# Performance work log

Hardware: AMD Instinct MI355X
Metric: run time of the kernel (lower is better)

## Reference

```python
import jax, jax.numpy as jnp
import numpy as np

# Mamba2 default hyperparameters
D_MODEL = 768
EXPAND = 2
D_STATE = 128
D_CONV = 4
HEADDIM = 64
D_INNER = EXPAND * D_MODEL            # 1536
NHEADS = D_INNER // HEADDIM           # 24
CONV_DIM = D_INNER + 2 * D_STATE      # 1792 (ngroups=1)
D_IN_PROJ = 2 * D_INNER + 2 * D_STATE + NHEADS  # 3352
B = 4
L = 2048
EPS = 1e-5


def setup_inputs() -> dict:
    key = jax.random.key(0)
    ks = jax.random.split(key, 8)
    return {
        "x": jax.random.normal(ks[0], (B, L, D_MODEL), jnp.float32),
        "in_proj_w": jax.random.normal(ks[1], (D_IN_PROJ, D_MODEL), jnp.float32) * 0.02,
        "conv_w": jax.random.normal(ks[2], (CONV_DIM, D_CONV), jnp.float32) * 0.2,
        "conv_b": jnp.zeros((CONV_DIM,), jnp.float32),
        # inverse-softplus of dt in [1e-3, 0.1] (Mamba2 dt init)
        "dt_bias": jnp.log(jnp.expm1(jax.random.uniform(ks[3], (NHEADS,), jnp.float32, 1e-3, 0.1))),
        "A_log": jnp.log(jax.random.uniform(ks[4], (NHEADS,), jnp.float32, 1.0, 16.0)),
        "D": jnp.ones((NHEADS,), jnp.float32),
        "norm_w": jnp.ones((D_INNER,), jnp.float32),
        "out_proj_w": jax.random.normal(ks[5], (D_MODEL, D_INNER), jnp.float32) * 0.02,
    }


def _mamba2(x, in_proj_w, conv_w, conv_b, dt_bias, A_log, D, norm_w, out_proj_w):
    b, l, _ = x.shape
    zxbcdt = x @ in_proj_w.T                              # (b,l,D_IN_PROJ)
    z, xBC, dt = jnp.split(zxbcdt, [D_INNER, D_INNER + CONV_DIM], axis=-1)

    # causal depthwise conv1d over channels of xBC, kernel D_CONV
    xp = jnp.pad(xBC, ((0, 0), (D_CONV - 1, 0), (0, 0)))
    conv = conv_b + sum(xp[:, k:k + l, :] * conv_w[:, k] for k in range(D_CONV))
    xBC = jax.nn.silu(conv)

    xh, Bm, Cm = jnp.split(xBC, [D_INNER, D_INNER + D_STATE], axis=-1)
    xh = xh.reshape(b, l, NHEADS, HEADDIM)               # (b,l,h,p)

    dt = jax.nn.softplus(dt + dt_bias)                   # (b,l,h)
    A = -jnp.exp(A_log)                                  # (h,)
    dA = jnp.exp(dt * A)                                 # (b,l,h)

    # selective SSM scan over time (state: (b,h,p,n))
    def step(state, inp):
        dA_t, dt_t, x_t, B_t, C_t = inp
        state = state * dA_t[:, :, None, None] \
              + (dt_t[:, :, None] * x_t)[..., None] * B_t[:, None, None, :]
        y_t = jnp.einsum('bhpn,bn->bhp', state, C_t)
        return state, y_t

    state0 = jnp.zeros((b, NHEADS, HEADDIM, D_STATE), x.dtype)
    xs = (dA.transpose(1, 0, 2), dt.transpose(1, 0, 2),
          xh.transpose(1, 0, 2, 3), Bm.transpose(1, 0, 2), Cm.transpose(1, 0, 2))
    _, ys = jax.lax.scan(step, state0, xs)               # (l,b,h,p)
    y = ys.transpose(1, 0, 2, 3) + D[:, None] * xh       # D skip connection
    y = y.reshape(b, l, D_INNER)

    # gated RMSNorm (norm_before_gate=False): normalize after gating by silu(z)
    y = y * jax.nn.silu(z)
    y = y * jax.lax.rsqrt(jnp.mean(y * y, axis=-1, keepdims=True) + EPS) * norm_w
    return y @ out_proj_w.T


def reference(x, in_proj_w, conv_w, conv_b, dt_bias, A_log, D, norm_w, out_proj_w):
    # MambaBlock.forward: Mamba2(x) + x
    return _mamba2(x, in_proj_w, conv_w, conv_b, dt_bias, A_log, D, norm_w, out_proj_w) + x
```

## Files before the change

### kernel.cpp

```cpp
#include <hip/hip_runtime.h>
#include <math.h>

typedef __bf16 bf16x8 __attribute__((ext_vector_type(8)));
typedef float  f32x4  __attribute__((ext_vector_type(4)));

#define QCHUNK 128
#define NCHUNK 16
#define SLD 136

__device__ __forceinline__ float bf2f(unsigned short u) {
    union { unsigned int i; float f; } v; v.i = ((unsigned int)u) << 16; return v.f;
}
__device__ __forceinline__ unsigned short f2bf(float f) {
    union { float f; unsigned int i; } v; v.f = f;
    unsigned int x = v.i;
    unsigned int r = (x + 0x7FFFu + ((x >> 16) & 1u)) >> 16;
    return (unsigned short)r;
}
__device__ __forceinline__ uint4 pack8(float4 a, float4 b) {
    uint4 r;
    r.x = (unsigned)f2bf(a.x) | ((unsigned)f2bf(a.y) << 16);
    r.y = (unsigned)f2bf(a.z) | ((unsigned)f2bf(a.w) << 16);
    r.z = (unsigned)f2bf(b.x) | ((unsigned)f2bf(b.y) << 16);
    r.w = (unsigned)f2bf(b.z) | ((unsigned)f2bf(b.w) << 16);
    return r;
}
__device__ __forceinline__ void load_lds16(const void* g, void* l) {
    __builtin_amdgcn_global_load_lds((const __attribute__((address_space(1))) void*)g,
                                     (__attribute__((address_space(3))) void*)l,
                                     16, 0, 0);
}

__global__ __launch_bounds__(256)
void convert_kernel(const float* __restrict__ x, const float* __restrict__ w_in,
                    const float* __restrict__ w_out,
                    unsigned short* __restrict__ x_bf, unsigned short* __restrict__ w_in_bf,
                    unsigned short* __restrict__ w_out_bf) {
    int idx = blockIdx.x * 256 + threadIdx.x;
    const int NX  = 8192 * 768 / 8;
    const int NW1 = 3328 * 768 / 8;
    const int NW2 = 768 * 1536 / 8;
    if (idx < NX) {
        const float* s = x + (size_t)idx * 8;
        *(uint4*)(x_bf + (size_t)idx * 8) = pack8(*(const float4*)s, *(const float4*)(s + 4));
    } else if (idx < NX + NW1) {
        int j = idx - NX;
        const float* s = w_in + (size_t)j * 8;
        *(uint4*)(w_in_bf + (size_t)j * 8) = pack8(*(const float4*)s, *(const float4*)(s + 4));
    } else if (idx < NX + NW1 + NW2) {
        int j = idx - NX - NW1;
        const float* s = w_out + (size_t)j * 8;
        *(uint4*)(w_out_bf + (size_t)j * 8) = pack8(*(const float4*)s, *(const float4*)(s + 4));
    }
}

__global__ __launch_bounds__(512)
void gemm_8phase(const unsigned short* __restrict__ A,
                 const unsigned short* __restrict__ Bw,
                 unsigned short* __restrict__ Out,
                 int ldo, int K) {
    extern __shared__ __align__(16) char smem[];

    const int tid = threadIdx.x;
    const int bid = blockIdx.x;
    const int xcd = bid & 7, local = bid >> 3;
    const int mt = xcd * 4 + local / 13;
    const int nt = local % 13;
    const int m0 = mt * 256, n0 = nt * 256;

    const int wave = tid >> 6, lane = tid & 63;
    const int wr = wave >> 2, wc = wave & 3;
    const int lr = lane & 15, q = lane >> 4;

    const int gl   = (lr & 7) << 4;
    const int arow = wr * 128 + lr;
    const int brow = wc * 64 + lr;
    const int colq = q << 4;

    const int srow  = tid >> 3;
    const int sslot = (tid & 7) ^ (srow & 7);
    const unsigned short* ga = A  + (size_t)(m0 + srow) * K + sslot * 8;
    const unsigned short* gb = Bw + (size_t)(n0 + srow) * K + sslot * 8;
    char* sAd = smem +         (size_t)tid * 16;
    char* sBd = smem + 65536 + (size_t)tid * 16;
    const size_t gstep = (size_t)64 * K;

    const int NT = K >> 6;
    f32x4 acc[8][4] = {};

    #pragma unroll
    for (int i = 0; i < 4; ++i) {
        load_lds16(ga + (size_t)i * gstep, sAd + i * 8192);
        load_lds16(gb + (size_t)i * gstep, sBd + i * 8192);
    }

    for (int t = 0; t < NT; ++t) {
        const int d = t & 1;
        const bool more = (t + 1 < NT);
        if (more) {
            const size_t kg = (size_t)(t + 1) * 64;
            const int ld = (d ^ 1) * 32768;
            #pragma unroll
            for (int i = 0; i < 4; ++i) {
                load_lds16(ga + kg + (size_t)i * gstep, sAd + ld + i * 8192);
                load_lds16(gb + kg + (size_t)i * gstep, sBd + ld + i * 8192);
            }
            asm volatile("s_waitcnt vmcnt(8)" ::: "memory");
        } else {
            asm volatile("s_waitcnt vmcnt(0)" ::: "memory");
        }
        __builtin_amdgcn_s_barrier();

        const char* pa = smem +         d * 32768;
        const char* pb = smem + 65536 + d * 32768;
        #pragma unroll
        for (int kh = 0; kh < 2; ++kh) {
            const int col = ((kh << 6) | colq) ^ gl;
            bf16x8 af[8], bfr[4];
            #pragma unroll
            for (int m = 0; m < 8; ++m)
                af[m] = *(const bf16x8*)(pa + (arow + m * 16) * 128 + col);
            #pragma unroll
            for (int n = 0; n < 4; ++n)
                bfr[n] = *(const bf16x8*)(pb + (brow + n * 16) * 128 + col);

            __builtin_amdgcn_s_setprio(1);
            #pragma unroll
            for (int m = 0; m < 8; ++m)
                #pragma unroll
                for (int n = 0; n < 4; ++n)
                    acc[m][n] = __builtin_amdgcn_mfma_f32_16x16x32_bf16(af[m], bfr[n], acc[m][n], 0, 0, 0);
            __builtin_amdgcn_s_setprio(0);
        }
        __builtin_amdgcn_s_barrier();
    }

    #pragma unroll
    for (int m = 0; m < 8; ++m) {
        #pragma unroll
        for (int r = 0; r < 4; ++r) {
            int row = m0 + wr * 128 + m * 16 + q * 4 + r;
            #pragma unroll
            for (int n = 0; n < 4; ++n) {
                int col = n0 + wc * 64 + n * 16 + lr;
                Out[(size_t)row * ldo + col] = f2bf(acc[m][n][r]);
            }
        }
    }
}

__global__ __launch_bounds__(512)
void gemm_out(const unsigned short* __restrict__ A,
              const unsigned short* __restrict__ Bw,
              float* __restrict__ Out, const float* __restrict__ Resid,
              int lda) {
    extern __shared__ __align__(16) char smem[];
    const int K = 1536, Nn = 768;

    const int tid = threadIdx.x;
    const int bid = blockIdx.x;
    const int xcd = bid & 7, local = bid >> 3;
    const int mt = xcd * 8 + local / 6;
    const int nt = local % 6;
    const int m0 = mt * 128, n0 = nt * 128;

    const int wave = tid >> 6, lane = tid & 63;
    const int wr = wave >> 2, wc = wave & 3;
    const int lr = lane & 15, q = lane >> 4;

    const int gl   = (lr & 7) << 4;
    const int arow = wr * 64 + lr;
    const int brow = wc * 32 + lr;
    const int colq = q << 4;

    const int srow  = tid >> 3;
    const int sslot = (tid & 7) ^ (srow & 7);
    const unsigned short* ga = A  + (size_t)(m0 + srow) * lda + sslot * 8;
    const unsigned short* gb = Bw + (size_t)(n0 + srow) * K   + sslot * 8;
    char* sAd = smem +         (size_t)tid * 16;
    char* sBd = smem + 32768 + (size_t)tid * 16;
    const size_t gstep_a = (size_t)64 * lda;
    const size_t gstep_b = (size_t)64 * K;

    f32x4 acc[4][2] = {};

    #pragma unroll
    for (int i = 0; i < 2; ++i) {
        load_lds16(ga + (size_t)i * gstep_a, sAd + i * 8192);
        load_lds16(gb + (size_t)i * gstep_b, sBd + i * 8192);
    }

    const int NT = K >> 6;
    for (int t = 0; t < NT; ++t) {
        const int d = t & 1;
        const bool more = (t + 1 < NT);
        if (more) {
            const size_t kg = (size_t)(t + 1) * 64;
            const int ld = (d ^ 1) * 16384;
            #pragma unroll
            for (int i = 0; i < 2; ++i) {
                load_lds16(ga + kg + (size_t)i * gstep_a, sAd + ld + i * 8192);
                load_lds16(gb + kg + (size_t)i * gstep_b, sBd + ld + i * 8192);
            }
            asm volatile("s_waitcnt vmcnt(4)" ::: "memory");
        } else {
            asm volatile("s_waitcnt vmcnt(0)" ::: "memory");
        }
        __builtin_amdgcn_s_barrier();

        const char* pa = smem +         d * 16384;
        const char* pb = smem + 32768 + d * 16384;
        #pragma unroll
        for (int kh = 0; kh < 2; ++kh) {
            const int col = ((kh << 6) | colq) ^ gl;
            bf16x8 af[4], bfr[2];
            #pragma unroll
            for (int m = 0; m < 4; ++m)
                af[m] = *(const bf16x8*)(pa + (arow + m * 16) * 128 + col);
            #pragma unroll
            for (int n = 0; n < 2; ++n)
                bfr[n] = *(const bf16x8*)(pb + (brow + n * 16) * 128 + col);

            __builtin_amdgcn_s_setprio(1);
            #pragma unroll
            for (int m = 0; m < 4; ++m)
                #pragma unroll
                for (int n = 0; n < 2; ++n)
                    acc[m][n] = __builtin_amdgcn_mfma_f32_16x16x32_bf16(af[m], bfr[n], acc[m][n], 0, 0, 0);
            __builtin_amdgcn_s_setprio(0);
        }
        __builtin_amdgcn_s_barrier();
    }

    #pragma unroll
    for (int m = 0; m < 4; ++m) {
        #pragma unroll
        for (int r = 0; r < 4; ++r) {
            int row = m0 + wr * 64 + m * 16 + q * 4 + r;
            #pragma unroll
            for (int n = 0; n < 2; ++n) {
                int col = n0 + wc * 32 + n * 16 + lr;
                Out[(size_t)row * Nn + col] = acc[m][n][r] + Resid[(size_t)row * Nn + col];
            }
        }
    }
}

__global__ __launch_bounds__(256)
void conv_fused_kernel(const unsigned short* __restrict__ zx,
                       const float* __restrict__ cw, const float* __restrict__ cb,
                       unsigned short* __restrict__ xT, unsigned short* __restrict__ bT,
                       unsigned short* __restrict__ Brow, unsigned short* __restrict__ Crow) {
    __shared__ unsigned short outt[64][66];
    __shared__ float cwl[64][4];
    __shared__ float cbl[64];

    int blk = blockIdx.x;
    int cht = blk % 28;
    int tt  = (blk / 28) % 32;
    int b   = blk / (28 * 32);
    int ch0 = cht * 64, t0 = tt * 64;
    int tid = threadIdx.x;
    int tx = tid & 63, ty = tid >> 6;

    if (tid < 64) cbl[tid] = cb[ch0 + tid];
    cwl[tid >> 2][tid & 3] = cw[(ch0 + (tid >> 2)) * 4 + (tid & 3)];
    __syncthreads();

    const unsigned short* zp = zx + (size_t)(b * 2048) * 3352 + 1536 + ch0 + tx;
    float w0 = cwl[tx][0], w1 = cwl[tx][1], w2 = cwl[tx][2], w3 = cwl[tx][3];
    float bias = cbl[tx];
    int tg = t0 + ty * 16;
    float r0 = (tg >= 3) ? bf2f(zp[(size_t)(tg - 3) * 3352]) : 0.f;
    float r1 = (tg >= 2) ? bf2f(zp[(size_t)(tg - 2) * 3352]) : 0.f;
    float r2 = (tg >= 1) ? bf2f(zp[(size_t)(tg - 1) * 3352]) : 0.f;
    #pragma unroll
    for (int k = 0; k < 16; ++k) {
        float cur = bf2f(zp[(size_t)(tg + k) * 3352]);
        float a = bias + r0 * w0 + r1 * w1 + r2 * w2 + cur * w3;
        a = a / (1.f + __expf(-a));
        outt[ty * 16 + k][tx] = f2bf(a);
        r0 = r1; r1 = r2; r2 = cur;
    }
    __syncthreads();

    if (ch0 < 1536) {
        unsigned short* dst = xT + ((size_t)(b * 1536 + ch0)) * 2048 + t0;
        #pragma unroll
        for (int k = 0; k < 16; ++k) {
            int chl = ty * 16 + k;
            dst[(size_t)chl * 2048 + tx] = outt[tx][chl];
        }
    } else if (ch0 < 1664) {
        int n0 = ch0 - 1536;
        unsigned short* dstT = bT + ((size_t)(b * 128 + n0)) * 2048 + t0;
        #pragma unroll
        for (int k = 0; k < 16; ++k) {
            int chl = ty * 16 + k;
            dstT[(size_t)chl * 2048 + tx] = outt[tx][chl];
        }
        unsigned short* dstR = Brow + ((size_t)(b * 2048 + t0)) * 128 + n0;
        int tl = tid >> 3, c8 = (tid & 7) << 3;
        #pragma unroll
        for (int it = 0; it < 2; ++it) {
            int t = tl + it * 32;
            unsigned short tmp[8];
            #pragma unroll
            for (int jj = 0; jj < 8; ++jj) tmp[jj] = outt[t][c8 + jj];
            *(uint4*)(dstR + (size_t)t * 128 + c8) = *(uint4*)tmp;
        }
    } else {
        int n0 = ch0 - 1664;
        unsigned short* dstR = Crow + ((size_t)(b * 2048 + t0)) * 128 + n0;
        int tl = tid >> 3, c8 = (tid & 7) << 3;
        #pragma unroll
        for (int it = 0; it < 2; ++it) {
            int t = tl + it * 32;
            unsigned short tmp[8];
            #pragma unroll
            for (int jj = 0; jj < 8; ++jj) tmp[jj] = outt[t][c8 + jj];
            *(uint4*)(dstR + (size_t)t * 128 + c8) = *(uint4*)tmp;
        }
    }
}

__global__ __launch_bounds__(256)
void dt_kernel(const float* __restrict__ x, const float* __restrict__ w_in,
               const float* __restrict__ dt_bias, const float* __restrict__ A_log,
               float2* __restrict__ dtdA) {
    __shared__ float xs[8 * 768];
    __shared__ float wsh[24 * 257];
    const int tid = threadIdx.x;
    const int row0 = blockIdx.x * 8;

    for (int i = tid; i < 8 * 768 / 4; i += 256)
        *(float4*)(xs + i * 4) = *(const float4*)(x + (size_t)row0 * 768 + (size_t)i * 4);

    const int rr = tid / 24, hh = tid - rr * 24;
    float acc0 = 0.f, acc1 = 0.f, acc2 = 0.f, acc3 = 0.f;

    for (int kc = 0; kc < 3; ++kc) {
        __syncthreads();
        for (int i = tid; i < 24 * 256; i += 256) {
            int h = i >> 8, kk = i & 255;
            wsh[h * 257 + kk] = w_in[(size_t)(3328 + h) * 768 + kc * 256 + kk];
        }
        __syncthreads();
        if (tid < 192) {
            const float* xp = xs + rr * 768 + kc * 256;
            const float* wp = wsh + hh * 257;
            #pragma unroll 16
            for (int kk = 0; kk < 256; kk += 4) {
                acc0 += xp[kk]     * wp[kk];
                acc1 += xp[kk + 1] * wp[kk + 1];
                acc2 += xp[kk + 2] * wp[kk + 2];
                acc3 += xp[kk + 3] * wp[kk + 3];
            }
        }
    }
    if (tid < 192) {
        float v = (acc0 + acc1) + (acc2 + acc3) + dt_bias[hh];
        float dt = (v > 20.f) ? v : log1pf(expf(v));
        float A = -expf(A_log[hh]);
        dtdA[(size_t)(row0 + rr) * 24 + hh] = make_float2(dt, dt * A);
    }
}

__global__ __launch_bounds__(256)
void ssd_local_kernel(const unsigned short* __restrict__ Brow,
                      const unsigned short* __restrict__ Crow,
                      const float2* __restrict__ dtdA,
                      const unsigned short* __restrict__ xT,
                      const unsigned short* __restrict__ bT,
                      const float* __restrict__ Dh,
                      unsigned short* __restrict__ yb,
                      unsigned short* __restrict__ sst,
                      float* __restrict__ Pbuf) {
    extern __shared__ __align__(16) char smem[];
    __bf16* Bs  = (__bf16*)smem;
    __bf16* Cs  = (__bf16*)(smem + 34816);
    float*  Lc  = (float*)(smem + 69632);
    float*  dtl = (float*)(smem + 70144);

    const int tid = threadIdx.x;
    const int c   = blockIdx.x & 15;
    const int bh  = blockIdx.x >> 4;
    const int b   = bh / 24, h = bh % 24;
    const int t0g = b * 2048 + c * QCHUNK;
    const int wave = tid >> 6, lane = tid & 63;
    const int lr = lane & 15, q = lane >> 4;

    for (int cc = tid; cc < 2048; cc += 256) {
        int r = cc >> 4, c8 = (cc & 15) << 3;
        *(uint4*)(Bs + r * SLD + c8) = *(const uint4*)(Brow + ((size_t)(t0g + r)) * 128 + c8);
        *(uint4*)(Cs + r * SLD + c8) = *(const uint4*)(Crow + ((size_t)(t0g + r)) * 128 + c8);
    }
    if (tid < 128) {
        float2 dd = dtdA[((size_t)t0g + tid) * 24 + h];
        dtl[tid] = dd.x;
        Lc[tid]  = dd.y;
    }
    __syncthreads();
    if (tid < 64) {
        float a0 = Lc[2 * tid], a1 = Lc[2 * tid + 1];
        float s = a0 + a1;
        #pragma unroll
        for (int d = 1; d < 64; d <<= 1) {
            float v = __shfl_up(s, d);
            if (tid >= d) s += v;
        }
        float ex = s - (a0 + a1);
        Lc[2 * tid]     = ex + a0;
        Lc[2 * tid + 1] = ex + a0 + a1;
    }
    __syncthreads();

    const int wm = (wave & 1) * 64, wn = (wave >> 1) * 64;
    f32x4 g[4][4] = {};
    #pragma unroll
    for (int k0 = 0; k0 < 128; k0 += 32) {
        bf16x8 af[4], bfr[4];
        #pragma unroll
        for (int t = 0; t < 4; ++t) {
            af[t]  = *(const bf16x8*)(Cs + (wm + t * 16 + lr) * SLD + k0 + q * 8);
            bfr[t] = *(const bf16x8*)(Bs + (wn + t * 16 + lr) * SLD + k0 + q * 8);
        }
        #pragma unroll
        for (int ti = 0; ti < 4; ++ti)
            #pragma unroll
            for (int tj = 0; tj < 4; ++tj)
                g[ti][tj] = __builtin_amdgcn_mfma_f32_16x16x32_bf16(af[ti], bfr[tj], g[ti][tj], 0, 0, 0);
    }
    __syncthreads();

    __bf16* Ms = Cs;
    {
        float lt_[4], dt_[4];
        #pragma unroll
        for (int tj = 0; tj < 4; ++tj) {
            int tau = wn + tj * 16 + lr;
            lt_[tj] = Lc[tau];
            dt_[tj] = dtl[tau];
        }
        #pragma unroll
        for (int ti = 0; ti < 4; ++ti) {
            #pragma unroll
            for (int r = 0; r < 4; ++r) {
                int t = wm + ti * 16 + q * 4 + r;
                float Lt = Lc[t];
                #pragma unroll
                for (int tj = 0; tj < 4; ++tj) {
                    int tau = wn + tj * 16 + lr;
                    float mv = (tau <= t) ? g[ti][tj][r] * __expf(Lt - lt_[tj]) * dt_[tj] : 0.f;
                    unsigned short u = f2bf(mv);
                    Ms[t * SLD + tau] = *(__bf16*)&u;
                }
            }
        }
    }

    __bf16* Xt  = Bs;
    __bf16* Xtw = (__bf16*)(smem + 17408);
    {
        float LQ = Lc[127];
        const unsigned short* xTb = xT + ((size_t)(b * 1536 + h * 64)) * 2048 + c * QCHUNK;
        for (int cc = tid; cc < 1024; cc += 256) {
            int p = cc >> 4, c8 = (cc & 15) << 3;
            uint4 v = *(const uint4*)(xTb + (size_t)p * 2048 + c8);
            *(uint4*)(Xt + p * SLD + c8) = v;
            unsigned short uu[8] = {(unsigned short)(v.x & 0xFFFF), (unsigned short)(v.x >> 16),
                                    (unsigned short)(v.y & 0xFFFF), (unsigned short)(v.y >> 16),
                                    (unsigned short)(v.z & 0xFFFF), (unsigned short)(v.z >> 16),
                                    (unsigned short)(v.w & 0xFFFF), (unsigned short)(v.w >> 16)};
            float w0[8];
            #pragma unroll
            for (int jj = 0; jj < 8; ++jj) {
                int tau = c8 + jj;
                w0[jj] = bf2f(uu[jj]) * __expf(LQ - Lc[tau]) * dtl[tau];
            }
            *(uint4*)(Xtw + p * SLD + c8) = pack8(make_float4(w0[0], w0[1], w0[2], w0[3]),
                                                  make_float4(w0[4], w0[5], w0[6], w0[7]));
        }
    }
    __syncthreads();

    {
        f32x4 so[2][4] = {};
        const unsigned short* bTb = bT + ((size_t)(b * 128)) * 2048 + c * QCHUNK;
        #pragma unroll
        for (int k0 = 0; k0 < 128; k0 += 32) {
            bf16x8 af[2], bfr[4];
            #pragma unroll
            for (int ti = 0; ti < 2; ++ti) {
                int n = wave * 32 + ti * 16 + lr;
                af[ti] = *(const bf16x8*)(bTb + (size_t)n * 2048 + k0 + q * 8);
            }
            #pragma unroll
            for (int tj = 0; tj < 4; ++tj)
                bfr[tj] = *(const bf16x8*)(Xtw + (tj * 16 + lr) * SLD + k0 + q * 8);
            #pragma unroll
            for (int ti = 0; ti < 2; ++ti)
                #pragma unroll
                for (int tj = 0; tj < 4; ++tj)
                    so[ti][tj] = __builtin_amdgcn_mfma_f32_16x16x32_bf16(af[ti], bfr[tj], so[ti][tj], 0, 0, 0);
        }
        unsigned short* sb = sst + ((size_t)(bh * NCHUNK + c)) * 8192;
        #pragma unroll
        for (int ti = 0; ti < 2; ++ti) {
            #pragma unroll
            for (int r = 0; r < 4; ++r) {
                int n = wave * 32 + ti * 16 + q * 4 + r;
                #pragma unroll
                for (int tj = 0; tj < 4; ++tj) {
                    int p = tj * 16 + lr;
                    sb[n * 64 + p] = f2bf(so[ti][tj][r]);
                }
            }
        }
        if (tid == 0) Pbuf[bh * NCHUNK + c] = __expf(Lc[127]);
    }

    {
        f32x4 ya[2][4] = {};
        #pragma unroll
        for (int k0 = 0; k0 < 128; k0 += 32) {
            bf16x8 af[2], bfr[4];
            #pragma unroll
            for (int ti = 0; ti < 2; ++ti)
                af[ti] = *(const bf16x8*)(Ms + (wave * 32 + ti * 16 + lr) * SLD + k0 + q * 8);
            #pragma unroll
            for (int tj = 0; tj < 4; ++tj)
                bfr[tj] = *(const bf16x8*)(Xt + (tj * 16 + lr) * SLD + k0 + q * 8);
            #pragma unroll
            for (int ti = 0; ti < 2; ++ti)
                #pragma unroll
                for (int tj = 0; tj < 4; ++tj)
                    ya[ti][tj] = __builtin_amdgcn_mfma_f32_16x16x32_bf16(af[ti], bfr[tj], ya[ti][tj], 0, 0, 0);
        }
        float Dv = Dh[h];
        unsigned short* ybb = yb + (size_t)t0g * 1536 + h * 64;
        #pragma unroll
        for (int ti = 0; ti < 2; ++ti) {
            #pragma unroll
            for (int r = 0; r < 4; ++r) {
                int t = wave * 32 + ti * 16 + q * 4 + r;
                #pragma unroll
                for (int tj = 0; tj < 4; ++tj) {
                    int p = tj * 16 + lr;
                    __bf16 xb = Xt[p * SLD + t];
                    float xv = bf2f(*(unsigned short*)&xb);
                    ybb[(size_t)t * 1536 + p] = f2bf(ya[ti][tj][r] + Dv * xv);
                }
            }
        }
    }
}

__global__ __launch_bounds__(256)
void combine_kernel(const unsigned short* __restrict__ sst,
                    unsigned short* __restrict__ sstT,
                    const float* __restrict__ Pbuf) {
    __shared__ unsigned short tl[32 * 130];
    const int blk = blockIdx.x;
    const int bh = blk >> 1;
    const int ph = (blk & 1) * 32;
    const int tid = threadIdx.x;
    const int pl = tid & 31;
    const int nb = tid >> 5;
    const unsigned short* sb = sst + (size_t)bh * NCHUNK * 8192;
    unsigned short* tb = sstT + (size_t)bh * NCHUNK * 8192 + ph * 128;
    const float* Pb = Pbuf + bh * NCHUNK;

    float s[16];
    #pragma unroll
    for (int i = 0; i < 16; ++i) s[i] = 0.f;

    for (int c = 0; c < NCHUNK; ++c) {
        const float Pc = Pb[c];
        const unsigned short* sc = sb + (size_t)c * 8192;
        #pragma unroll
        for (int i = 0; i < 16; ++i) {
            int n = nb + 8 * i;
            unsigned short v = sc[n * 64 + ph + pl];
            tl[pl * 130 + n] = f2bf(s[i]);
            s[i] = Pc * s[i] + bf2f(v);
        }
        __syncthreads();
        uint* tlw = (uint*)tl;
        uint4* tc4 = (uint4*)(tb + (size_t)c * 8192);
        #pragma unroll
        for (int k = 0; k < 2; ++k) {
            int j = tid + k * 256;
            int pp = j >> 4;
            int w0 = pp * 65 + (j & 15) * 4;
            tc4[j] = make_uint4(tlw[w0], tlw[w0 + 1], tlw[w0 + 2], tlw[w0 + 3]);
        }
        __syncthreads();
    }
}

__global__ __launch_bounds__(256)
void ssd_inter_kernel(const unsigned short* __restrict__ Crow,
                      const float2* __restrict__ dtdA,
                      const unsigned short* __restrict__ sstT,
                      unsigned short* __restrict__ yb) {
    __shared__ __align__(16) __bf16 Cs[128 * SLD];
    __shared__ __align__(16) __bf16 St[64 * SLD];
    __shared__ float Lc[128];

    const int tid = threadIdx.x;
    const int blk = blockIdx.x;
    const int bh = blk / 15;
    const int c  = blk % 15 + 1;
    const int b = bh / 24, h = bh % 24;
    const int t0g = b * 2048 + c * QCHUNK;
    const int wave = tid >> 6, lane = tid & 63;
    const int lr = lane & 15, q = lane >> 4;

    for (int cc = tid; cc < 2048; cc += 256) {
        int r = cc >> 4, c8 = (cc & 15) << 3;
        *(uint4*)(Cs + r * SLD + c8) = *(const uint4*)(Crow + ((size_t)(t0g + r)) * 128 + c8);
    }
    const unsigned short* stb = sstT + ((size_t)(bh * NCHUNK + c)) * 8192;
    for (int cc = tid; cc < 1024; cc += 256) {
        int p = cc >> 4, c8 = (cc & 15) << 3;
        *(uint4*)(St + p * SLD + c8) = *(const uint4*)(stb + p * 128 + c8);
    }
    if (tid < 128) Lc[tid] = dtdA[((size_t)t0g + tid) * 24 + h].y;
    __syncthreads();
    if (tid < 64) {
        float a0 = Lc[2 * tid], a1 = Lc[2 * tid + 1];
        float s = a0 + a1;
        #pragma unroll
        for (int d = 1; d < 64; d <<= 1) {
            float v = __shfl_up(s, d);
            if (tid >= d) s += v;
        }
        float ex = s - (a0 + a1);
        Lc[2 * tid]     = ex + a0;
        Lc[2 * tid + 1] = ex + a0 + a1;
    }
    __syncthreads();

    f32x4 ya[2][4] = {};
    #pragma unroll
    for (int k0 = 0; k0 < 128; k0 += 32) {
        bf16x8 af[2], bfr[4];
        #pragma unroll
        for (int ti = 0; ti < 2; ++ti)
            af[ti] = *(const bf16x8*)(Cs + (wave * 32 + ti * 16 + lr) * SLD + k0 + q * 8);
        #pragma unroll
        for (int tj = 0; tj < 4; ++tj)
            bfr[tj] = *(const bf16x8*)(St + (tj * 16 + lr) * SLD + k0 + q * 8);
        #pragma unroll
        for (int ti = 0; ti < 2; ++ti)
            #pragma unroll
            for (int tj = 0; tj < 4; ++tj)
                ya[ti][tj] = __builtin_amdgcn_mfma_f32_16x16x32_bf16(af[ti], bfr[tj], ya[ti][tj], 0, 0, 0);
    }
    unsigned short* ybb = yb + (size_t)t0g * 1536 + h * 64;
    #pragma unroll
    for (int ti = 0; ti < 2; ++ti) {
        #pragma unroll
        for (int r = 0; r < 4; ++r) {
            int t = wave * 32 + ti * 16 + q * 4 + r;
            float sc = __expf(Lc[t]);
            #pragma unroll
            for (int tj = 0; tj < 4; ++tj) {
                int p = tj * 16 + lr;
                unsigned short* yp = ybb + (size_t)t * 1536 + p;
                *yp = f2bf(bf2f(*yp) + sc * ya[ti][tj][r]);
            }
        }
    }
}

__global__ __launch_bounds__(256)
void norm_kernel(const unsigned short* __restrict__ yb,
                 unsigned short* __restrict__ zx,
                 const float* __restrict__ nw) {
    int row = blockIdx.x;
    const unsigned short* yr = yb + (size_t)row * 1536;
    unsigned short* zr = zx + (size_t)row * 3352;
    int tid = threadIdx.x;
    float u[6];
    float ss = 0.f;
    #pragma unroll
    for (int i = 0; i < 6; ++i) {
        int c = tid + i * 256;
        float z = bf2f(zr[c]);
        float uu = bf2f(yr[c]) * (z / (1.f + __expf(-z)));
        u[i] = uu;
        ss += uu * uu;
    }
    #pragma unroll
    for (int m = 1; m < 64; m <<= 1) ss += __shfl_xor(ss, m);
    __shared__ float red[4];
    if ((tid & 63) == 0) red[tid >> 6] = ss;
    __syncthreads();
    float tot = red[0] + red[1] + red[2] + red[3];
    float inv = rsqrtf(tot * (1.f / 1536.f) + 1e-5f);
    #pragma unroll
    for (int i = 0; i < 6; ++i) {
        int c = tid + i * 256;
        zr[1536 + c] = f2bf(u[i] * inv * nw[c]);
    }
}

extern "C" void kernel_launch(void* const* d_in, const int* in_sizes, int n_in,
                              void* d_out, int out_size, void* d_ws, size_t ws_size,
                              hipStream_t stream) {
    const float* x       = (const float*)d_in[0];
    const float* w_in    = (const float*)d_in[1];
    const float* conv_w  = (const float*)d_in[2];
    const float* conv_b  = (const float*)d_in[3];
    const float* dt_bias = (const float*)d_in[4];
    const float* A_log   = (const float*)d_in[5];
    const float* Dp      = (const float*)d_in[6];
    const float* nw      = (const float*)d_in[7];
    const float* w_out   = (const float*)d_in[8];
    float* out = (float*)d_out;

    char* ws = (char*)d_ws;
    const size_t off_zx   = 0;
    const size_t off_A    = off_zx + 54919168;
    const size_t off_xT   = off_A;
    const size_t off_bT   = off_A + 25165824;
    const size_t off_Brow = off_A + 27262976;
    const size_t off_Crow = off_A + 29360128;
    const size_t off_dtdA = off_A + 58720256;
    const size_t off_y    = off_dtdA + 1572864;
    const size_t off_sst  = off_y + 50331648;
    const size_t off_P    = off_sst + 25165824;

    unsigned short* zx   = (unsigned short*)(ws + off_zx);
    unsigned short* xT   = (unsigned short*)(ws + off_xT);
    unsigned short* bT   = (unsigned short*)(ws + off_bT);
    unsigned short* Brow = (unsigned short*)(ws + off_Brow);
    unsigned short* Crow = (unsigned short*)(ws + off_Crow);
    float2* dtdA = (float2*)(ws + off_dtdA);
    unsigned short* yb   = (unsigned short*)(ws + off_y);
    unsigned short* sst  = (unsigned short*)(ws + off_sst);
    unsigned short* sstT = xT;
    float* Pbuf = (float*)(ws + off_P);

    unsigned short* x_bf     = (unsigned short*)(ws + off_y);
    unsigned short* w_out_bf = (unsigned short*)(ws + off_y + 25165824);
    unsigned short* w_in_bf  = (unsigned short*)(ws + off_sst);

    static bool attr_set = false;
    if (!attr_set) {
        hipFuncSetAttribute((const void*)ssd_local_kernel,
                            hipFuncAttributeMaxDynamicSharedMemorySize, 70656);
        hipFuncSetAttribute((const void*)gemm_8phase,
                            hipFuncAttributeMaxDynamicSharedMemorySize, 131072);
        hipFuncSetAttribute((const void*)gemm_out,
                            hipFuncAttributeMaxDynamicSharedMemorySize, 65536);
        attr_set = true;
    }

    convert_kernel<<<4896, 256, 0, stream>>>(x, w_in, w_out, x_bf, w_in_bf, w_out_bf);
    gemm_8phase<<<416, 512, 131072, stream>>>(x_bf, w_in_bf, zx, 3352, 768);
    conv_fused_kernel<<<3584, 256, 0, stream>>>(zx, conv_w, conv_b, xT, bT, Brow, Crow);
    dt_kernel<<<1024, 256, 0, stream>>>(x, w_in, dt_bias, A_log, dtdA);
    ssd_local_kernel<<<1536, 256, 70656, stream>>>(Brow, Crow, dtdA, xT, bT, Dp, yb, sst, Pbuf);
    combine_kernel<<<192, 256, 0, stream>>>(sst, sstT, Pbuf);
    ssd_inter_kernel<<<1440, 256, 0, stream>>>(Crow, dtdA, sstT, yb);
    norm_kernel<<<8192, 256, 0, stream>>>(yb, zx, nw);
    gemm_out<<<384, 512, 65536, stream>>>(zx + 1536, w_out_bf, out, x, 3352);
}
```

Before: 318.9 us.

## Shrink SSD local kernel LDS by staging B in halves and folding decay weights into bT

Cuts the ssd_local_kernel shared memory from about 69KB to 53KB. B is now staged in two 64-column halves through a smaller buffer, and the CB^T GEMM is split into two K passes with an extra sync between them. The separate decay-weighted X tile in LDS is dropped; the exp(LQ-L)*dt weights are applied in registers to the bT fragments loaded from global. The goal is to fit more blocks per CU, at the cost of extra syncs and the weight exp computed redundantly per wave.

```diff
diff --git a/kernel.cpp b/kernel.cpp
--- a/kernel.cpp
+++ b/kernel.cpp
@@ -7,6 +7,7 @@
 #define QCHUNK 128
 #define NCHUNK 16
 #define SLD 136
+#define SLDB 72
 
 __device__ __forceinline__ float bf2f(unsigned short u) {
     union { unsigned int i; float f; } v; v.i = ((unsigned int)u) << 16; return v.f;
@@ -377,10 +378,10 @@
                       unsigned short* __restrict__ sst,
                       float* __restrict__ Pbuf) {
     extern __shared__ __align__(16) char smem[];
-    __bf16* Bs  = (__bf16*)smem;
-    __bf16* Cs  = (__bf16*)(smem + 34816);
-    float*  Lc  = (float*)(smem + 69632);
-    float*  dtl = (float*)(smem + 70144);
+    __bf16* Bh  = (__bf16*)smem;
+    __bf16* Cs  = (__bf16*)(smem + 18432);
+    float*  Lc  = (float*)(smem + 53248);
+    float*  dtl = (float*)(smem + 53760);
 
     const int tid = threadIdx.x;
     const int c   = blockIdx.x & 15;
@@ -392,8 +393,11 @@
 
     for (int cc = tid; cc < 2048; cc += 256) {
         int r = cc >> 4, c8 = (cc & 15) << 3;
-        *(uint4*)(Bs + r * SLD + c8) = *(const uint4*)(Brow + ((size_t)(t0g + r)) * 128 + c8);
         *(uint4*)(Cs + r * SLD + c8) = *(const uint4*)(Crow + ((size_t)(t0g + r)) * 128 + c8);
+    }
+    for (int cc = tid; cc < 1024; cc += 256) {
+        int r = cc >> 3, c8 = (cc & 7) << 3;
+        *(uint4*)(Bh + r * SLDB + c8) = *(const uint4*)(Brow + ((size_t)(t0g + r)) * 128 + c8);
     }
     if (tid < 128) {
         float2 dd = dtdA[((size_t)t0g + tid) * 24 + h];
@@ -401,6 +405,7 @@
         Lc[tid]  = dd.y;
     }
     __syncthreads();
+
     if (tid < 64) {
         float a0 = Lc[2 * tid], a1 = Lc[2 * tid + 1];
         float s = a0 + a1;
@@ -413,17 +418,36 @@
         Lc[2 * tid]     = ex + a0;
         Lc[2 * tid + 1] = ex + a0 + a1;
     }
-    __syncthreads();
 
     const int wm = (wave & 1) * 64, wn = (wave >> 1) * 64;
     f32x4 g[4][4] = {};
     #pragma unroll
-    for (int k0 = 0; k0 < 128; k0 += 32) {
+    for (int k0 = 0; k0 < 64; k0 += 32) {
         bf16x8 af[4], bfr[4];
         #pragma unroll
         for (int t = 0; t < 4; ++t) {
             af[t]  = *(const bf16x8*)(Cs + (wm + t * 16 + lr) * SLD + k0 + q * 8);
-            bfr[t] = *(const bf16x8*)(Bs + (wn + t * 16 + lr) * SLD + k0 + q * 8);
+            bfr[t] = *(const bf16x8*)(Bh + (wn + t * 16 + lr) * SLDB + k0 + q * 8);
+        }
+        #pragma unroll
+        for (int ti = 0; ti < 4; ++ti)
+            #pragma unroll
+            for (int tj = 0; tj < 4; ++tj)
+                g[ti][tj] = __builtin_amdgcn_mfma_f32_16x16x32_bf16(af[ti], bfr[tj], g[ti][tj], 0, 0, 0);
+    }
+    __syncthreads();
+    for (int cc = tid; cc < 1024; cc += 256) {
+        int r = cc >> 3, c8 = (cc & 7) << 3;
+        *(uint4*)(Bh + r * SLDB + c8) = *(const uint4*)(Brow + ((size_t)(t0g + r)) * 128 + 64 + c8);
+    }
+    __syncthreads();
+    #pragma unroll
+    for (int k0 = 0; k0 < 64; k0 += 32) {
+        bf16x8 af[4], bfr[4];
+        #pragma unroll
+        for (int t = 0; t < 4; ++t) {
+            af[t]  = *(const bf16x8*)(Cs + (wm + t * 16 + lr) * SLD + 64 + k0 + q * 8);
+            bfr[t] = *(const bf16x8*)(Bh + (wn + t * 16 + lr) * SLDB + k0 + q * 8);
         }
         #pragma unroll
         for (int ti = 0; ti < 4; ++ti)
@@ -459,45 +483,40 @@
         }
     }
 
-    __bf16* Xt  = Bs;
-    __bf16* Xtw = (__bf16*)(smem + 17408);
+    __bf16* Xt = Bh;
     {
-        float LQ = Lc[127];
         const unsigned short* xTb = xT + ((size_t)(b * 1536 + h * 64)) * 2048 + c * QCHUNK;
         for (int cc = tid; cc < 1024; cc += 256) {
             int p = cc >> 4, c8 = (cc & 15) << 3;
-            uint4 v = *(const uint4*)(xTb + (size_t)p * 2048 + c8);
-            *(uint4*)(Xt + p * SLD + c8) = v;
-            unsigned short uu[8] = {(unsigned short)(v.x & 0xFFFF), (unsigned short)(v.x >> 16),
-                                    (unsigned short)(v.y & 0xFFFF), (unsigned short)(v.y >> 16),
-                                    (unsigned short)(v.z & 0xFFFF), (unsigned short)(v.z >> 16),
-                                    (unsigned short)(v.w & 0xFFFF), (unsigned short)(v.w >> 16)};
-            float w0[8];
-            #pragma unroll
-            for (int jj = 0; jj < 8; ++jj) {
-                int tau = c8 + jj;
-                w0[jj] = bf2f(uu[jj]) * __expf(LQ - Lc[tau]) * dtl[tau];
-            }
-            *(uint4*)(Xtw + p * SLD + c8) = pack8(make_float4(w0[0], w0[1], w0[2], w0[3]),
-                                                  make_float4(w0[4], w0[5], w0[6], w0[7]));
+            *(uint4*)(Xt + p * SLD + c8) = *(const uint4*)(xTb + (size_t)p * 2048 + c8);
         }
     }
     __syncthreads();
 
     {
+        float LQ = Lc[127];
         f32x4 so[2][4] = {};
         const unsigned short* bTb = bT + ((size_t)(b * 128)) * 2048 + c * QCHUNK;
         #pragma unroll
         for (int k0 = 0; k0 < 128; k0 += 32) {
+            float w0[8];
+            #pragma unroll
+            for (int jj = 0; jj < 8; ++jj) {
+                int tau = k0 + q * 8 + jj;
+                w0[jj] = __expf(LQ - Lc[tau]) * dtl[tau];
+            }
             bf16x8 af[2], bfr[4];
             #pragma unroll
             for (int ti = 0; ti < 2; ++ti) {
                 int n = wave * 32 + ti * 16 + lr;
-                af[ti] = *(const bf16x8*)(bTb + (size_t)n * 2048 + k0 + q * 8);
+                bf16x8 raw = *(const bf16x8*)(bTb + (size_t)n * 2048 + k0 + q * 8);
+                #pragma unroll
+                for (int jj = 0; jj < 8; ++jj)
+                    af[ti][jj] = (__bf16)((float)raw[jj] * w0[jj]);
             }
             #pragma unroll
             for (int tj = 0; tj < 4; ++tj)
-                bfr[tj] = *(const bf16x8*)(Xtw + (tj * 16 + lr) * SLD + k0 + q * 8);
+                bfr[tj] = *(const bf16x8*)(Xt + (tj * 16 + lr) * SLD + k0 + q * 8);
             #pragma unroll
             for (int ti = 0; ti < 2; ++ti)
                 #pragma unroll
@@ -751,7 +770,7 @@
     static bool attr_set = false;
     if (!attr_set) {
         hipFuncSetAttribute((const void*)ssd_local_kernel,
-                            hipFuncAttributeMaxDynamicSharedMemorySize, 70656);
+                            hipFuncAttributeMaxDynamicSharedMemorySize, 54272);
         hipFuncSetAttribute((const void*)gemm_8phase,
                             hipFuncAttributeMaxDynamicSharedMemorySize, 131072);
         hipFuncSetAttribute((const void*)gemm_out,
@@ -763,7 +782,7 @@
     gemm_8phase<<<416, 512, 131072, stream>>>(x_bf, w_in_bf, zx, 3352, 768);
     conv_fused_kernel<<<3584, 256, 0, stream>>>(zx, conv_w, conv_b, xT, bT, Brow, Crow);
     dt_kernel<<<1024, 256, 0, stream>>>(x, w_in, dt_bias, A_log, dtdA);
-    ssd_local_kernel<<<1536, 256, 70656, stream>>>(Brow, Crow, dtdA, xT, bT, Dp, yb, sst, Pbuf);
+    ssd_local_kernel<<<1536, 256, 54272, stream>>>(Brow, Crow, dtdA, xT, bT, Dp, yb, sst, Pbuf);
     combine_kernel<<<192, 256, 0, stream>>>(sst, sstT, Pbuf);
     ssd_inter_kernel<<<1440, 256, 0, stream>>>(Crow, dtdA, sstT, yb);
     norm_kernel<<<8192, 256, 0, stream>>>(yb, zx, nw);
```

Measured after the change: 320.8 us. About the same (+0.6%).
